# Performance work log

Hardware: AMD Instinct MI355X
Metric: run time of the kernel (lower is better)

Reference implementation:

```python
import jax, jax.numpy as jnp
import numpy as np

N, C, O, H, S, SHARE = 30000, 128, 128, 8, 16, 8
D = O // H            # mid_planes = 16
OS = O // SHARE       # 16
OFFSETS = [15000, 30000]
EPS = 1e-5


def _knn(p, offsets, k):
    """Exact per-batch KNN (incl. self), chunked to bound memory."""
    n = p.shape[0]
    idx = np.empty((n, k), dtype=np.int64)
    start = 0
    for end in offsets:
        pb = p[start:end]
        sq = (pb * pb).sum(-1)
        for qs in range(0, pb.shape[0], 1024):
            q = pb[qs:qs + 1024]
            d = sq[qs:qs + q.shape[0], None] - 2.0 * (q @ pb.T) + sq[None, :]
            part = np.argpartition(d, k - 1, axis=1)[:, :k]
            idx[start + qs:start + qs + q.shape[0]] = part + start
        start = end
    return idx


def _ln(x, g, b):
    m = x.mean(-1, keepdims=True)
    v = ((x - m) ** 2).mean(-1, keepdims=True)
    return (x - m) / jnp.sqrt(v + EPS) * g + b


def setup_inputs() -> dict:
    rng = np.random.default_rng(0)
    p_np = (rng.standard_normal((N, 3)) * 5.0).astype(np.float32)
    idx = _knn(p_np, OFFSETS, S)

    key = jax.random.key(0)
    ks = jax.random.split(key, 12)

    def lin(k, i, o):
        return (jax.random.normal(k, (i, o), jnp.float32) / np.sqrt(i)).astype(jnp.float32)

    return {
        "p": jnp.asarray(p_np),
        "x": jax.random.normal(ks[0], (N, C), jnp.float32),
        "idx": jnp.asarray(idx),
        "Wq": lin(ks[1], C, O), "bq": jnp.zeros((O,), jnp.float32),
        "Wk": lin(ks[2], C, O), "bk": jnp.zeros((O,), jnp.float32),
        "Wv": lin(ks[3], C, O), "bv": jnp.zeros((O,), jnp.float32),
        "Wp1": lin(ks[4], 3, 3), "bp1": jnp.zeros((3,), jnp.float32),
        "gp": jnp.ones((3,), jnp.float32), "betap": jnp.zeros((3,), jnp.float32),
        "Wp2": lin(ks[5], 3, O), "bp2": jnp.zeros((O,), jnp.float32),
        "gw1": jnp.ones((D,), jnp.float32), "betaw1": jnp.zeros((D,), jnp.float32),
        "Ww1": lin(ks[6], D, OS), "bw1": jnp.zeros((OS,), jnp.float32),
        "gw2": jnp.ones((OS,), jnp.float32), "betaw2": jnp.zeros((OS,), jnp.float32),
        "Ww2": lin(ks[7], OS, OS), "bw2": jnp.zeros((OS,), jnp.float32),
    }


def reference(p, x, idx, Wq, bq, Wk, bk, Wv, bv, Wp1, bp1, gp, betap, Wp2, bp2,
              gw1, betaw1, Ww1, bw1, gw2, betaw2, Ww2, bw2):
    xq = (x @ Wq + bq).reshape(N, H, D)          # (N,H,D)
    xk = x @ Wk + bk                              # (N,O)
    xv = x @ Wv + bv
    kg = xk[idx].reshape(N, S, H, D)              # neighbor gather
    vg = xv[idx].reshape(N, S, H, D)
    pr = p[idx] - p[:, None, :]                   # relative coords (N,S,3)
    pe = jax.nn.relu(_ln(pr @ Wp1 + bp1, gp, betap)) @ Wp2 + bp2  # (N,S,O)
    pe = pe.reshape(N, S, H, D)
    r = kg + pe - xq[:, None]                     # (N,S,H,D)
    w = jax.nn.relu(_ln(r, gw1, betaw1)) @ Ww1 + bw1
    w = jax.nn.relu(_ln(w, gw2, betaw2)) @ Ww2 + bw2  # (N,S,H,OS)
    w = jax.nn.softmax(w.mean(-1), axis=1)        # softmax over the S neighbors
    out = ((vg + pe) * w[..., None]).sum(axis=1)  # weighted neighbor reduce
    return out.reshape(N, O)
```

## Files before the change

kernel.cpp:

```cpp
#include <hip/hip_runtime.h>
#include <math.h>

typedef unsigned int  uint;
typedef unsigned short ushort;

constexpr int NPTS = 30000;
constexpr int CIN  = 128;
constexpr int OC   = 128;
constexpr int NH   = 8;
constexpr int NS   = 16;
constexpr int DH   = 16;
constexpr int OSH  = 16;
constexpr float EPSF = 1e-5f;

typedef __attribute__((ext_vector_type(8))) short bf16x8;
typedef __attribute__((ext_vector_type(4))) float f32x4;
typedef __attribute__((ext_vector_type(2))) __fp16 h16x2;

__device__ __forceinline__ ushort f2bf(float f) {
    uint u = __float_as_uint(f);
    u += 0x7fff + ((u >> 16) & 1);
    return (ushort)(u >> 16);
}
__device__ __forceinline__ void bf2f2(uint u, float& f0, float& f1) {
    f0 = __uint_as_float(u << 16);
    f1 = __uint_as_float(u & 0xffff0000u);
}

#if defined(__has_builtin)
#if __has_builtin(__builtin_amdgcn_fdot2)
#define HAVE_FDOT2 1
#endif
#endif

constexpr int LDK = 72;

__global__ __launch_bounds__(256) void qkv_mfma(
    const float* __restrict__ x,
    const float* __restrict__ Wq, const float* __restrict__ Wk, const float* __restrict__ Wv,
    const float* __restrict__ bq, const float* __restrict__ bk, const float* __restrict__ bv,
    const float* __restrict__ Ww1, const float* __restrict__ Ww2, const float* __restrict__ bw2,
    ushort* __restrict__ yq, ushort* __restrict__ yk, ushort* __restrict__ yv,
    uint* __restrict__ Ww1p, float* __restrict__ rmean)
{
    const int mat = blockIdx.y;
    const float* W    = (mat == 0) ? Wq : (mat == 1 ? Wk : Wv);
    const float* bias = (mat == 0) ? bq : (mat == 1 ? bk : bv);
    ushort* y         = (mat == 0) ? yq : (mat == 1 ? yk : yv);

    const int n0 = blockIdx.x * 128;
    const int t  = threadIdx.x;

    if (blockIdx.x == 0 && mat == 0) {
        if (t < 128) {
            int d2 = t >> 4, o2 = t & 15;
            h16x2 pk = __builtin_amdgcn_cvt_pkrtz(Ww1[(2 * d2) * OSH + o2],
                                                  Ww1[(2 * d2 + 1) * OSH + o2]);
            Ww1p[t] = *(uint*)&pk;
        } else if (t >= 128 && t < 144) {
            int d = t - 128;
            float acc = 0.f;
            #pragma unroll
            for (int o2 = 0; o2 < OSH; ++o2) acc += Ww2[d * OSH + o2];
            rmean[d] = acc * (1.f / OSH);
        } else if (t == 144) {
            float acc = 0.f;
            #pragma unroll
            for (int o2 = 0; o2 < OSH; ++o2) acc += bw2[o2];
            rmean[OSH] = acc * (1.f / OSH);
        }
    }

    __shared__ ushort As[128 * LDK];
    __shared__ ushort Bs[128 * LDK];

    const int wave = t >> 6;
    const int lane = t & 63;
    const int m16  = lane & 15;
    const int quad = lane >> 4;

    f32x4 acc[2][8];
    #pragma unroll
    for (int mt = 0; mt < 2; ++mt)
        #pragma unroll
        for (int nt = 0; nt < 8; ++nt)
            acc[mt][nt] = (f32x4){0.f, 0.f, 0.f, 0.f};

    const int arow0 = wave * 32 + m16;

    for (int kh = 0; kh < 2; ++kh) {
        const int k0 = kh * 64;
        #pragma unroll
        for (int i = 0; i < 4; ++i) {
            int c   = t + 256 * i;
            int row = c >> 3;
            int off = c & 7;
            int gr  = n0 + row;
            uint4 u = make_uint4(0, 0, 0, 0);
            if (gr < NPTS) {
                const float* src = x + (size_t)gr * CIN + k0 + off * 8;
                float4 f0 = *(const float4*)(src);
                float4 f1 = *(const float4*)(src + 4);
                u.x = (uint)f2bf(f0.x) | ((uint)f2bf(f0.y) << 16);
                u.y = (uint)f2bf(f0.z) | ((uint)f2bf(f0.w) << 16);
                u.z = (uint)f2bf(f1.x) | ((uint)f2bf(f1.y) << 16);
                u.w = (uint)f2bf(f1.z) | ((uint)f2bf(f1.w) << 16);
            }
            *(uint4*)&As[row * LDK + off * 8] = u;
        }
        #pragma unroll
        for (int i = 0; i < 8; ++i) {
            int fidx = t + 256 * i;
            int kl   = fidx >> 5;
            int o4   = fidx & 31;
            float4 w = *(const float4*)(W + (size_t)(k0 + kl) * OC + o4 * 4);
            Bs[(o4 * 4 + 0) * LDK + kl] = f2bf(w.x);
            Bs[(o4 * 4 + 1) * LDK + kl] = f2bf(w.y);
            Bs[(o4 * 4 + 2) * LDK + kl] = f2bf(w.z);
            Bs[(o4 * 4 + 3) * LDK + kl] = f2bf(w.w);
        }
        __syncthreads();

        #pragma unroll
        for (int ks = 0; ks < 2; ++ks) {
            const int kb = ks * 32 + quad * 8;
            bf16x8 a0 = *(const bf16x8*)&As[(arow0 +  0) * LDK + kb];
            bf16x8 a1 = *(const bf16x8*)&As[(arow0 + 16) * LDK + kb];
            #pragma unroll
            for (int nt = 0; nt < 8; ++nt) {
                bf16x8 b = *(const bf16x8*)&Bs[(nt * 16 + m16) * LDK + kb];
                acc[0][nt] = __builtin_amdgcn_mfma_f32_16x16x32_bf16(a0, b, acc[0][nt], 0, 0, 0);
                acc[1][nt] = __builtin_amdgcn_mfma_f32_16x16x32_bf16(a1, b, acc[1][nt], 0, 0, 0);
            }
        }
        __syncthreads();
    }

    #pragma unroll
    for (int mt = 0; mt < 2; ++mt) {
        #pragma unroll
        for (int nt = 0; nt < 8; ++nt) {
            const int col = nt * 16 + m16;
            const float bcol = bias[col];
            #pragma unroll
            for (int r = 0; r < 4; ++r) {
                int row = n0 + wave * 32 + mt * 16 + quad * 4 + r;
                if (row < NPTS)
                    y[(size_t)row * OC + col] = f2bf(acc[mt][nt][r] + bcol);
            }
        }
    }
}

__global__ __launch_bounds__(128) void attn_kernel(
    const float* __restrict__ p, const int* __restrict__ idx,
    const ushort* __restrict__ xq, const ushort* __restrict__ xk, const ushort* __restrict__ xv,
    const float* __restrict__ Wp1, const float* __restrict__ bp1,
    const float* __restrict__ gp,  const float* __restrict__ betap,
    const float* __restrict__ Wp2, const float* __restrict__ bp2,
    const float* __restrict__ gw1, const float* __restrict__ betaw1,
    const float* __restrict__ Ww1, const float* __restrict__ bw1,
    const float* __restrict__ gw2, const float* __restrict__ betaw2,
    const uint* __restrict__ Ww1p, const float* __restrict__ rmean,
    float* __restrict__ out)
{
    const int n = blockIdx.x;
    const int t = threadIdx.x;
    const int s = t >> 3;
    const int h = t & 7;

    __shared__ float s_t[NS][4];
    __shared__ float s_logit[NS][NH];
    __shared__ float s_mx[NH];
    __shared__ float s_inv[NH];
    __shared__ float s_contrib[NS][OC];

    if (t < NS) {
        int ss = t;
        int j = idx[n * NS + ss];
        float pr0 = p[j * 3 + 0] - p[n * 3 + 0];
        float pr1 = p[j * 3 + 1] - p[n * 3 + 1];
        float pr2 = p[j * 3 + 2] - p[n * 3 + 2];
        float u[3];
        #pragma unroll
        for (int c = 0; c < 3; ++c)
            u[c] = bp1[c] + pr0 * Wp1[0 * 3 + c] + pr1 * Wp1[1 * 3 + c] + pr2 * Wp1[2 * 3 + c];
        float m   = (u[0] + u[1] + u[2]) * (1.f / 3.f);
        float d0 = u[0] - m, d1 = u[1] - m, d2 = u[2] - m;
        float var = (d0 * d0 + d1 * d1 + d2 * d2) * (1.f / 3.f);
        float inv = rsqrtf(var + EPSF);
        #pragma unroll
        for (int c = 0; c < 3; ++c)
            s_t[ss][c] = fmaxf((u[c] - m) * inv * gp[c] + betap[c], 0.f);
    }
    __syncthreads();

    const int j = idx[n * NS + s];
    const float t0 = s_t[s][0], t1 = s_t[s][1], t2 = s_t[s][2];
    const int obase = h * DH;

    float pe[DH];
    #pragma unroll
    for (int d = 0; d < DH; ++d) {
        int o = obase + d;
        pe[d] = bp2[o] + t0 * Wp2[0 * OC + o] + t1 * Wp2[1 * OC + o] + t2 * Wp2[2 * OC + o];
    }

    float vv[DH], r[DH];
    {
        const uint4* k4 = (const uint4*)(xk + (size_t)j * OC + obase);
        const uint4* v4 = (const uint4*)(xv + (size_t)j * OC + obase);
        const uint4* q4 = (const uint4*)(xq + (size_t)n * OC + obase);
        uint4 ku0 = k4[0], ku1 = k4[1];
        uint4 vu0 = v4[0], vu1 = v4[1];
        uint4 qu0 = q4[0], qu1 = q4[1];
        float kf[DH], qf[DH];
        bf2f2(ku0.x, kf[0], kf[1]);   bf2f2(ku0.y, kf[2], kf[3]);
        bf2f2(ku0.z, kf[4], kf[5]);   bf2f2(ku0.w, kf[6], kf[7]);
        bf2f2(ku1.x, kf[8], kf[9]);   bf2f2(ku1.y, kf[10], kf[11]);
        bf2f2(ku1.z, kf[12], kf[13]); bf2f2(ku1.w, kf[14], kf[15]);
        bf2f2(vu0.x, vv[0], vv[1]);   bf2f2(vu0.y, vv[2], vv[3]);
        bf2f2(vu0.z, vv[4], vv[5]);   bf2f2(vu0.w, vv[6], vv[7]);
        bf2f2(vu1.x, vv[8], vv[9]);   bf2f2(vu1.y, vv[10], vv[11]);
        bf2f2(vu1.z, vv[12], vv[13]); bf2f2(vu1.w, vv[14], vv[15]);
        bf2f2(qu0.x, qf[0], qf[1]);   bf2f2(qu0.y, qf[2], qf[3]);
        bf2f2(qu0.z, qf[4], qf[5]);   bf2f2(qu0.w, qf[6], qf[7]);
        bf2f2(qu1.x, qf[8], qf[9]);   bf2f2(qu1.y, qf[10], qf[11]);
        bf2f2(qu1.z, qf[12], qf[13]); bf2f2(qu1.w, qf[14], qf[15]);
        #pragma unroll
        for (int d = 0; d < DH; ++d)
            r[d] = kf[d] + pe[d] - qf[d];
    }

    float a[DH];
    {
        float m = 0.f;
        #pragma unroll
        for (int d = 0; d < DH; ++d) m += r[d];
        m *= (1.f / DH);
        float var = 0.f;
        #pragma unroll
        for (int d = 0; d < DH; ++d) { float dd = r[d] - m; var += dd * dd; }
        var *= (1.f / DH);
        float inv = rsqrtf(var + EPSF);
        #pragma unroll
        for (int d = 0; d < DH; ++d)
            a[d] = fmaxf((r[d] - m) * inv * gw1[d] + betaw1[d], 0.f);
    }

    float w1[OSH];
    #pragma unroll
    for (int o2 = 0; o2 < OSH; ++o2) w1[o2] = bw1[o2];
#ifdef HAVE_FDOT2
    {
        h16x2 ap[8];
        #pragma unroll
        for (int d2 = 0; d2 < 8; ++d2)
            ap[d2] = __builtin_amdgcn_cvt_pkrtz(a[2 * d2], a[2 * d2 + 1]);
        #pragma unroll
        for (int d2 = 0; d2 < 8; ++d2) {
            #pragma unroll
            for (int o2 = 0; o2 < OSH; ++o2) {
                uint wp = Ww1p[d2 * OSH + o2];
                w1[o2] = __builtin_amdgcn_fdot2(ap[d2], *(h16x2*)&wp, w1[o2], false);
            }
        }
    }
#else
    #pragma unroll
    for (int d = 0; d < DH; ++d) {
        float av = a[d];
        #pragma unroll
        for (int o2 = 0; o2 < OSH; ++o2) w1[o2] = fmaf(av, Ww1[d * OSH + o2], w1[o2]);
    }
#endif

    float logit;
    {
        float m = 0.f;
        #pragma unroll
        for (int o2 = 0; o2 < OSH; ++o2) m += w1[o2];
        m *= (1.f / OSH);
        float var = 0.f;
        #pragma unroll
        for (int o2 = 0; o2 < OSH; ++o2) { float dd = w1[o2] - m; var += dd * dd; }
        var *= (1.f / OSH);
        float inv = rsqrtf(var + EPSF);
        logit = rmean[OSH];
        #pragma unroll
        for (int o2 = 0; o2 < OSH; ++o2) {
            float bv2 = fmaxf((w1[o2] - m) * inv * gw2[o2] + betaw2[o2], 0.f);
            logit = fmaf(bv2, rmean[o2], logit);
        }
    }

    s_logit[s][h] = logit;
    __syncthreads();

    if (t < NH) {
        float mx = -1e30f;
        #pragma unroll
        for (int ss = 0; ss < NS; ++ss) mx = fmaxf(mx, s_logit[ss][t]);
        float denom = 0.f;
        #pragma unroll
        for (int ss = 0; ss < NS; ++ss) denom += __expf(s_logit[ss][t] - mx);
        s_mx[t] = mx;
        s_inv[t] = 1.f / denom;
    }
    __syncthreads();

    float w = __expf(logit - s_mx[h]) * s_inv[h];

    #pragma unroll
    for (int d = 0; d < DH; ++d)
        s_contrib[s][obase + d] = (vv[d] + pe[d]) * w;
    __syncthreads();

    float acc = 0.f;
    #pragma unroll
    for (int ss = 0; ss < NS; ++ss) acc += s_contrib[ss][t];
    out[(size_t)n * OC + t] = acc;
}

extern "C" void kernel_launch(void* const* d_in, const int* in_sizes, int n_in,
                              void* d_out, int out_size, void* d_ws, size_t ws_size,
                              hipStream_t stream) {
    const float* p     = (const float*)d_in[0];
    const float* x     = (const float*)d_in[1];
    const int*   idx   = (const int*)d_in[2];
    const float* Wq    = (const float*)d_in[3];
    const float* bq    = (const float*)d_in[4];
    const float* Wk    = (const float*)d_in[5];
    const float* bk    = (const float*)d_in[6];
    const float* Wv    = (const float*)d_in[7];
    const float* bv    = (const float*)d_in[8];
    const float* Wp1   = (const float*)d_in[9];
    const float* bp1   = (const float*)d_in[10];
    const float* gp    = (const float*)d_in[11];
    const float* betap = (const float*)d_in[12];
    const float* Wp2   = (const float*)d_in[13];
    const float* bp2   = (const float*)d_in[14];
    const float* gw1   = (const float*)d_in[15];
    const float* betaw1= (const float*)d_in[16];
    const float* Ww1   = (const float*)d_in[17];
    const float* bw1   = (const float*)d_in[18];
    const float* gw2   = (const float*)d_in[19];
    const float* betaw2= (const float*)d_in[20];
    const float* Ww2   = (const float*)d_in[21];
    const float* bw2   = (const float*)d_in[22];
    float* out = (float*)d_out;

    ushort* xq = (ushort*)d_ws;
    ushort* xk = xq + (size_t)NPTS * OC;
    ushort* xv = xk + (size_t)NPTS * OC;
    uint*   Ww1p  = (uint*)(xv + (size_t)NPTS * OC);
    float*  rmean = (float*)(Ww1p + 128);

    dim3 g1((NPTS + 127) / 128, 3);
    qkv_mfma<<<g1, 256, 0, stream>>>(x, Wq, Wk, Wv, bq, bk, bv,
                                     Ww1, Ww2, bw2,
                                     xq, xk, xv, Ww1p, rmean);

    attn_kernel<<<NPTS, 128, 0, stream>>>(p, idx, xq, xk, xv,
                                          Wp1, bp1, gp, betap, Wp2, bp2,
                                          gw1, betaw1, Ww1, bw1,
                                          gw2, betaw2, Ww1p, rmean, out);
}
```

Before: 225.7 us.

## Precompute bf16 x and transposed weights in a prep kernel, drop LDS staging in QKV GEMM

```diff
diff --git a/kernel.cpp b/kernel.cpp
--- a/kernel.cpp
+++ b/kernel.cpp
@@ -5,6 +5,7 @@
 typedef unsigned short ushort;
 
 constexpr int NPTS = 30000;
+constexpr int NPAD = 30080;
 constexpr int CIN  = 128;
 constexpr int OC   = 128;
 constexpr int NH   = 8;
@@ -33,25 +34,36 @@
 #endif
 #endif
 
-constexpr int LDK = 72;
-
-__global__ __launch_bounds__(256) void qkv_mfma(
+constexpr int XB_BLOCKS = (NPAD * CIN / 4) / 256;
+
+__global__ __launch_bounds__(256) void prep_kernel(
     const float* __restrict__ x,
     const float* __restrict__ Wq, const float* __restrict__ Wk, const float* __restrict__ Wv,
-    const float* __restrict__ bq, const float* __restrict__ bk, const float* __restrict__ bv,
     const float* __restrict__ Ww1, const float* __restrict__ Ww2, const float* __restrict__ bw2,
-    ushort* __restrict__ yq, ushort* __restrict__ yk, ushort* __restrict__ yv,
+    ushort* __restrict__ xb, ushort* __restrict__ WT,
     uint* __restrict__ Ww1p, float* __restrict__ rmean)
 {
-    const int mat = blockIdx.y;
-    const float* W    = (mat == 0) ? Wq : (mat == 1 ? Wk : Wv);
-    const float* bias = (mat == 0) ? bq : (mat == 1 ? bk : bv);
-    ushort* y         = (mat == 0) ? yq : (mat == 1 ? yk : yv);
-
-    const int n0 = blockIdx.x * 128;
-    const int t  = threadIdx.x;
-
-    if (blockIdx.x == 0 && mat == 0) {
+    const int b = blockIdx.x;
+    const int t = threadIdx.x;
+    if (b < XB_BLOCKS) {
+        int e   = (b * 256 + t) * 4;
+        int row = e >> 7;
+        uint2 o = make_uint2(0, 0);
+        if (row < NPTS) {
+            float4 f = *(const float4*)(x + e);
+            o.x = (uint)f2bf(f.x) | ((uint)f2bf(f.y) << 16);
+            o.y = (uint)f2bf(f.z) | ((uint)f2bf(f.w) << 16);
+        }
+        *(uint2*)(xb + e) = o;
+    } else if (b < XB_BLOCKS + 3) {
+        int mat = b - XB_BLOCKS;
+        const float* W = (mat == 0) ? Wq : (mat == 1 ? Wk : Wv);
+        ushort* T = WT + mat * OC * CIN;
+        if (t < OC) {
+            for (int k = 0; k < CIN; ++k)
+                T[t * CIN + k] = f2bf(W[k * OC + t]);
+        }
+    } else {
         if (t < 128) {
             int d2 = t >> 4, o2 = t & 15;
             h16x2 pk = __builtin_amdgcn_cvt_pkrtz(Ww1[(2 * d2) * OSH + o2],
@@ -70,10 +82,20 @@
             rmean[OSH] = acc * (1.f / OSH);
         }
     }
-
-    __shared__ ushort As[128 * LDK];
-    __shared__ ushort Bs[128 * LDK];
-
+}
+
+__global__ __launch_bounds__(256) void qkv_mfma(
+    const ushort* __restrict__ xb, const ushort* __restrict__ WT,
+    const float* __restrict__ bq, const float* __restrict__ bk, const float* __restrict__ bv,
+    ushort* __restrict__ yq, ushort* __restrict__ yk, ushort* __restrict__ yv)
+{
+    const int mat = blockIdx.y;
+    const float* bias = (mat == 0) ? bq : (mat == 1 ? bk : bv);
+    ushort* y         = (mat == 0) ? yq : (mat == 1 ? yk : yv);
+    const ushort* T   = WT + mat * OC * CIN;
+
+    const int n0   = blockIdx.x * 128;
+    const int t    = threadIdx.x;
     const int wave = t >> 6;
     const int lane = t & 63;
     const int m16  = lane & 15;
@@ -86,54 +108,20 @@
         for (int nt = 0; nt < 8; ++nt)
             acc[mt][nt] = (f32x4){0.f, 0.f, 0.f, 0.f};
 
-    const int arow0 = wave * 32 + m16;
-
-    for (int kh = 0; kh < 2; ++kh) {
-        const int k0 = kh * 64;
-        #pragma unroll
-        for (int i = 0; i < 4; ++i) {
-            int c   = t + 256 * i;
-            int row = c >> 3;
-            int off = c & 7;
-            int gr  = n0 + row;
-            uint4 u = make_uint4(0, 0, 0, 0);
-            if (gr < NPTS) {
-                const float* src = x + (size_t)gr * CIN + k0 + off * 8;
-                float4 f0 = *(const float4*)(src);
-                float4 f1 = *(const float4*)(src + 4);
-                u.x = (uint)f2bf(f0.x) | ((uint)f2bf(f0.y) << 16);
-                u.y = (uint)f2bf(f0.z) | ((uint)f2bf(f0.w) << 16);
-                u.z = (uint)f2bf(f1.x) | ((uint)f2bf(f1.y) << 16);
-                u.w = (uint)f2bf(f1.z) | ((uint)f2bf(f1.w) << 16);
-            }
-            *(uint4*)&As[row * LDK + off * 8] = u;
-        }
-        #pragma unroll
-        for (int i = 0; i < 8; ++i) {
-            int fidx = t + 256 * i;
-            int kl   = fidx >> 5;
-            int o4   = fidx & 31;
-            float4 w = *(const float4*)(W + (size_t)(k0 + kl) * OC + o4 * 4);
-            Bs[(o4 * 4 + 0) * LDK + kl] = f2bf(w.x);
-            Bs[(o4 * 4 + 1) * LDK + kl] = f2bf(w.y);
-            Bs[(o4 * 4 + 2) * LDK + kl] = f2bf(w.z);
-            Bs[(o4 * 4 + 3) * LDK + kl] = f2bf(w.w);
-        }
-        __syncthreads();
-
-        #pragma unroll
-        for (int ks = 0; ks < 2; ++ks) {
-            const int kb = ks * 32 + quad * 8;
-            bf16x8 a0 = *(const bf16x8*)&As[(arow0 +  0) * LDK + kb];
-            bf16x8 a1 = *(const bf16x8*)&As[(arow0 + 16) * LDK + kb];
-            #pragma unroll
-            for (int nt = 0; nt < 8; ++nt) {
-                bf16x8 b = *(const bf16x8*)&Bs[(nt * 16 + m16) * LDK + kb];
-                acc[0][nt] = __builtin_amdgcn_mfma_f32_16x16x32_bf16(a0, b, acc[0][nt], 0, 0, 0);
-                acc[1][nt] = __builtin_amdgcn_mfma_f32_16x16x32_bf16(a1, b, acc[1][nt], 0, 0, 0);
-            }
-        }
-        __syncthreads();
+    const ushort* arow0 = xb + (size_t)(n0 + wave * 32 + m16) * CIN;
+    const ushort* arow1 = arow0 + 16 * CIN;
+
+    #pragma unroll
+    for (int ks = 0; ks < 4; ++ks) {
+        const int kb = ks * 32 + quad * 8;
+        bf16x8 a0 = *(const bf16x8*)(arow0 + kb);
+        bf16x8 a1 = *(const bf16x8*)(arow1 + kb);
+        #pragma unroll
+        for (int nt = 0; nt < 8; ++nt) {
+            bf16x8 bfr = *(const bf16x8*)(T + (size_t)(nt * 16 + m16) * CIN + kb);
+            acc[0][nt] = __builtin_amdgcn_mfma_f32_16x16x32_bf16(a0, bfr, acc[0][nt], 0, 0, 0);
+            acc[1][nt] = __builtin_amdgcn_mfma_f32_16x16x32_bf16(a1, bfr, acc[1][nt], 0, 0, 0);
+        }
     }
 
     #pragma unroll
@@ -173,7 +161,7 @@
     __shared__ float s_logit[NS][NH];
     __shared__ float s_mx[NH];
     __shared__ float s_inv[NH];
-    __shared__ float s_contrib[NS][OC];
+    __shared__ float s_contrib[NS][OC + 4];
 
     if (t < NS) {
         int ss = t;
@@ -200,10 +188,22 @@
     const int obase = h * DH;
 
     float pe[DH];
-    #pragma unroll
-    for (int d = 0; d < DH; ++d) {
-        int o = obase + d;
-        pe[d] = bp2[o] + t0 * Wp2[0 * OC + o] + t1 * Wp2[1 * OC + o] + t2 * Wp2[2 * OC + o];
+    {
+        const float* W0 = Wp2 + obase;
+        const float* W1 = Wp2 + OC + obase;
+        const float* W2 = Wp2 + 2 * OC + obase;
+        const float* B  = bp2 + obase;
+        #pragma unroll
+        for (int q = 0; q < 4; ++q) {
+            float4 a0 = *(const float4*)(W0 + q * 4);
+            float4 a1 = *(const float4*)(W1 + q * 4);
+            float4 a2 = *(const float4*)(W2 + q * 4);
+            float4 bb = *(const float4*)(B + q * 4);
+            pe[q * 4 + 0] = bb.x + t0 * a0.x + t1 * a1.x + t2 * a2.x;
+            pe[q * 4 + 1] = bb.y + t0 * a0.y + t1 * a1.y + t2 * a2.y;
+            pe[q * 4 + 2] = bb.z + t0 * a0.z + t1 * a1.z + t2 * a2.z;
+            pe[q * 4 + 3] = bb.w + t0 * a0.w + t1 * a1.w + t2 * a2.w;
+        }
     }
 
     float vv[DH], r[DH];
@@ -350,16 +350,19 @@
     const float* bw2   = (const float*)d_in[22];
     float* out = (float*)d_out;
 
-    ushort* xq = (ushort*)d_ws;
+    ushort* xb = (ushort*)d_ws;
+    ushort* WT = xb + (size_t)NPAD * CIN;
+    ushort* xq = WT + 3 * OC * CIN;
     ushort* xk = xq + (size_t)NPTS * OC;
     ushort* xv = xk + (size_t)NPTS * OC;
     uint*   Ww1p  = (uint*)(xv + (size_t)NPTS * OC);
     float*  rmean = (float*)(Ww1p + 128);
 
-    dim3 g1((NPTS + 127) / 128, 3);
-    qkv_mfma<<<g1, 256, 0, stream>>>(x, Wq, Wk, Wv, bq, bk, bv,
-                                     Ww1, Ww2, bw2,
-                                     xq, xk, xv, Ww1p, rmean);
+    prep_kernel<<<XB_BLOCKS + 4, 256, 0, stream>>>(x, Wq, Wk, Wv, Ww1, Ww2, bw2,
+                                                   xb, WT, Ww1p, rmean);
+
+    dim3 g1(NPAD / 128, 3);
+    qkv_mfma<<<g1, 256, 0, stream>>>(xb, WT, bq, bk, bv, xq, xk, xv);
 
     attn_kernel<<<NPTS, 128, 0, stream>>>(p, idx, xq, xk, xv,
                                           Wp1, bp1, gp, betap, Wp2, bp2,
```

Result: no change. 223.3 us (-1.1%).
